# Kernel tuning notes

Measured on AMD Instinct MI355X. Metric: run time of the kernel, lower is better.

The kernel has to match this reference:

```python
import jax, jax.numpy as jnp
import numpy as np

B, C, H, W = 4, 256, 96, 96
HEADS, RATE = 8, 1


def setup_inputs() -> dict:
    key = jax.random.key(0)
    ks = [jax.random.fold_in(key, i) for i in range(8)]
    kpe = 2 * (RATE // 2) + 1  # PE depthwise kernel size (1 for rate=1)
    return {
        "q": jax.random.normal(ks[0], (B, C, H, W), jnp.float32),
        "k": jax.random.normal(ks[1], (B, C, H, W), jnp.float32),
        "v": jax.random.normal(ks[2], (B, C, H, W), jnp.float32),
        "wq": jax.random.normal(ks[3], (C, C), jnp.float32) * 0.02,          # q_proj 1x1 (used for q,k,v per source)
        "pe_dw": jax.random.normal(ks[4], (9, 1, kpe, kpe), jnp.float32) * 0.3,  # grouped conv, groups=9
        "pe_pw": jax.random.normal(ks[5], (9, 9, 1, 1), jnp.float32) * 0.3,      # 1x1 mixing conv
        "wo": jax.random.normal(ks[6], (C, C), jnp.float32) * 0.02,          # out_proj weight
        "bo": jax.random.normal(ks[7], (C,), jnp.float32) * 0.02,            # out_proj bias
    }


def _unfold3(x, rate):
    # torch.nn.Unfold(3, dilation=rate, padding=rate) then view(N, c, 9, H, W)
    # kernel positions are row-major (ki, kj), channel-major layout -> stack on axis 2.
    n, c, h, w = x.shape
    xp = jnp.pad(x, ((0, 0), (0, 0), (rate, rate), (rate, rate)))
    pats = [xp[:, :, i * rate:i * rate + h, j * rate:j * rate + w]
            for i in range(3) for j in range(3)]
    return jnp.stack(pats, axis=2)  # (N, c, 9, H, W)


def reference(q, b_unused_k=None, v=None, wq=None, pe_dw=None, pe_pw=None, wo=None, bo=None, k=None):
    raise NotImplementedError  # replaced below


def reference(q, k, v, wq, pe_dw, pe_pw, wo, bo):
    b = q.shape[0]
    ch = C // HEADS
    proj = lambda x: jnp.einsum('oc,bchw->bohw', wq, x)  # source uses q_proj for q, k AND v
    qh = proj(q).reshape(b * HEADS, ch, H, W)
    kh = proj(k).reshape(b * HEADS, ch, H, W)
    vh = proj(v).reshape(b * HEADS, ch, H, W)

    ku = _unfold3(kh, RATE)                              # (bH, ch, 9, H, W)
    f = jnp.einsum('nchw,nckhw->nkhw', qh, ku)           # per-pixel 3x3 scores (bH, 9, H, W)

    pad = RATE // 2
    dn = ('NCHW', 'OIHW', 'NCHW')
    f = jax.lax.conv_general_dilated(f, pe_dw, (1, 1), [(pad, pad), (pad, pad)],
                                     feature_group_count=9, dimension_numbers=dn)
    f = jax.lax.conv_general_dilated(f, pe_pw, (1, 1), 'VALID', dimension_numbers=dn)
    s = jax.nn.softmax(f, axis=1)                        # softmax over 9 kernel positions

    vu = _unfold3(vh, RATE)                              # (bH, ch, 9, H, W)
    o = jnp.einsum('nckhw,nkhw->nchw', vu, s).reshape(b, C, H, W)
    return jnp.einsum('oc,bchw->bohw', wo, o) + bo[None, :, None, None]
```

## Files before the change

### kernel.cpp

```cpp
#include <hip/hip_runtime.h>
#include <math.h>

#define HH 96
#define WW 96
#define PP 9216
#define CCH 256
#define BB 4
#define CH 32

typedef unsigned short u16;
typedef short bf16x8 __attribute__((ext_vector_type(8)));
typedef float f32x4 __attribute__((ext_vector_type(4)));

__device__ __forceinline__ float bf2f(unsigned s) { return __uint_as_float(s << 16); }
__device__ __forceinline__ u16 f2bf(float f) {
  unsigned u = __float_as_uint(f);
  return (u16)((u + 0x7fffu + ((u >> 16) & 1u)) >> 16);
}

typedef __attribute__((address_space(1))) const unsigned int GUI;
typedef __attribute__((address_space(3))) unsigned int LUI;
__device__ __forceinline__ void gload16(const void* g, void* l) {
  __builtin_amdgcn_global_load_lds((GUI*)g, (LUI*)l, 16, 0, 0);
}

__global__ __launch_bounds__(256)
void wcvt(const float* __restrict__ wq, const float* __restrict__ wo,
          u16* __restrict__ Wbf) {
  int i = blockIdx.x * 256 + threadIdx.x;
  const float* s = (i < 16384) ? (wq + (size_t)i * 4) : (wo + (size_t)(i - 16384) * 4);
  float4 v = *(const float4*)s;
  uint2 u;
  u.x = (unsigned)f2bf(v.x) | ((unsigned)f2bf(v.y) << 16);
  u.y = (unsigned)f2bf(v.z) | ((unsigned)f2bf(v.w) << 16);
  *(uint2*)(Wbf + (size_t)i * 4) = u;
}

__global__ __launch_bounds__(256)
void gemm_qkvf(const float* __restrict__ qin, const float* __restrict__ kin,
               const float* __restrict__ vin, const u16* __restrict__ Wbf,
               u16* __restrict__ Xcl) {
  __shared__ u16 Wl[256 * 64];
  __shared__ u16 Xl[64 * 64];
  const int t = threadIdx.x;
  const int w = t >> 6, l = t & 63;
  const int lr = l & 15, lg = l >> 4;
  const int pblk = blockIdx.x * 64;
  const int z = blockIdx.z;
  const int b = z & 3, which = z >> 2;
  const float* Xf = ((which == 0) ? qin : (which == 1) ? kin : vin) + (size_t)b * CCH * PP;
  u16* Y = Xcl + (size_t)z * ((size_t)PP * CCH);

  f32x4 acc[4][4];
#pragma unroll
  for (int mi = 0; mi < 4; mi++)
#pragma unroll
    for (int ni = 0; ni < 4; ni++) acc[mi][ni] = (f32x4){0.f, 0.f, 0.f, 0.f};

  for (int kk = 0; kk < 4; kk++) {
    const int c0 = kk * 64;
#pragma unroll
    for (int i = 0; i < 8; i++) {
      int r0 = (w * 8 + i) * 8;
      int row = r0 + (l >> 3);
      int gs = (l & 7) ^ (row & 7);
      gload16(Wbf + (size_t)row * CCH + c0 + gs * 8, (void*)&Wl[r0 * 64]);
    }
    float4 xr[4];
#pragma unroll
    for (int rr = 0; rr < 4; rr++) {
      int cc = w * 4 + rr * 16 + lg;
      xr[rr] = *(const float4*)(Xf + (size_t)(c0 + cc) * PP + pblk + lr * 4);
    }
#pragma unroll
    for (int rr = 0; rr < 4; rr++) {
      float r0 = xr[rr].x, r1 = xr[rr].y, r2 = xr[rr].z, r3 = xr[rr].w;
      bool b0 = (lg & 1), b1 = (lg & 2);
      float s0 = b0 ? r0 : r1;
      float s1 = b0 ? r2 : r3;
      float u0 = __shfl_xor(s0, 16, 64);
      float u1 = __shfl_xor(s1, 16, 64);
      float m0 = b0 ? u0 : r0;
      float m1 = b0 ? r1 : u0;
      float m2 = b0 ? u1 : r2;
      float m3 = b0 ? r3 : u1;
      float s2 = b1 ? m0 : m2;
      float s3 = b1 ? m1 : m3;
      float w0 = __shfl_xor(s2, 32, 64);
      float w1 = __shfl_xor(s3, 32, 64);
      float o0 = b1 ? w0 : m0;
      float o1 = b1 ? w1 : m1;
      float o2 = b1 ? m2 : w0;
      float o3 = b1 ? m3 : w1;
      int cbase = w * 4 + rr * 16;
      int pl = lr * 4 + lg;
      int qg = cbase >> 3, h8 = (cbase >> 2) & 1;
      unsigned lo = (unsigned)f2bf(o0) | ((unsigned)f2bf(o1) << 16);
      unsigned hi = (unsigned)f2bf(o2) | ((unsigned)f2bf(o3) << 16);
      *(uint2*)(&Xl[pl * 64 + ((qg ^ (pl & 7)) << 3) + h8 * 4]) = make_uint2(lo, hi);
    }
    __syncthreads();
#pragma unroll
    for (int ks = 0; ks < 2; ks++) {
      const int g = ks * 4 + lg;
      bf16x8 wf[4], xf[4];
#pragma unroll
      for (int i = 0; i < 4; i++) {
        int row = w * 64 + i * 16 + lr;
        wf[i] = *(const bf16x8*)&Wl[row * 64 + ((g ^ (row & 7)) << 3)];
      }
#pragma unroll
      for (int i = 0; i < 4; i++) {
        int row = i * 16 + lr;
        xf[i] = *(const bf16x8*)&Xl[row * 64 + ((g ^ (row & 7)) << 3)];
      }
#pragma unroll
      for (int mi = 0; mi < 4; mi++)
#pragma unroll
        for (int ni = 0; ni < 4; ni++)
          acc[mi][ni] = __builtin_amdgcn_mfma_f32_16x16x32_bf16(
              wf[mi], xf[ni], acc[mi][ni], 0, 0, 0);
    }
    __syncthreads();
  }
#pragma unroll
  for (int mi = 0; mi < 4; mi++)
#pragma unroll
    for (int ni = 0; ni < 4; ni++) {
      int o = w * 64 + mi * 16 + lg * 4;
      int p = pblk + ni * 16 + lr;
      f32x4 a = acc[mi][ni];
      uint2 u;
      u.x = (unsigned)f2bf(a[0]) | ((unsigned)f2bf(a[1]) << 16);
      u.y = (unsigned)f2bf(a[2]) | ((unsigned)f2bf(a[3]) << 16);
      *(uint2*)(Y + (size_t)p * CCH + o) = u;
    }
}

__global__ __launch_bounds__(256)
void gemm_out_m(const u16* __restrict__ Xbuf, const u16* __restrict__ Wbf,
                const float* __restrict__ bias, float* __restrict__ outY) {
  __shared__ u16 Wl[256 * 64];
  __shared__ u16 Xl[64 * 64];
  const int t = threadIdx.x;
  const int w = t >> 6, l = t & 63;
  const int lr = l & 15, lg = l >> 4;
  const int pblk = blockIdx.x * 64;
  const int z = blockIdx.z;
  const u16* Xb = Xbuf + (size_t)z * ((size_t)PP * CCH);

  f32x4 acc[4][4];
#pragma unroll
  for (int mi = 0; mi < 4; mi++)
#pragma unroll
    for (int ni = 0; ni < 4; ni++) acc[mi][ni] = (f32x4){0.f, 0.f, 0.f, 0.f};

  for (int kk = 0; kk < 4; kk++) {
    const int c0 = kk * 64;
#pragma unroll
    for (int i = 0; i < 8; i++) {
      int r0 = (w * 8 + i) * 8;
      int row = r0 + (l >> 3);
      int gs = (l & 7) ^ (row & 7);
      gload16(Wbf + (size_t)row * CCH + c0 + gs * 8, (void*)&Wl[r0 * 64]);
    }
#pragma unroll
    for (int i = 0; i < 2; i++) {
      int r0 = (w * 2 + i) * 8;
      int row = r0 + (l >> 3);
      int gs = (l & 7) ^ (row & 7);
      gload16(Xb + (size_t)(pblk + row) * CCH + c0 + gs * 8, (void*)&Xl[r0 * 64]);
    }
    __syncthreads();
#pragma unroll
    for (int ks = 0; ks < 2; ks++) {
      const int g = ks * 4 + lg;
      bf16x8 wf[4], xf[4];
#pragma unroll
      for (int i = 0; i < 4; i++) {
        int row = w * 64 + i * 16 + lr;
        wf[i] = *(const bf16x8*)&Wl[row * 64 + ((g ^ (row & 7)) << 3)];
      }
#pragma unroll
      for (int i = 0; i < 4; i++) {
        int row = i * 16 + lr;
        xf[i] = *(const bf16x8*)&Xl[row * 64 + ((g ^ (row & 7)) << 3)];
      }
#pragma unroll
      for (int mi = 0; mi < 4; mi++)
#pragma unroll
        for (int ni = 0; ni < 4; ni++)
          acc[mi][ni] = __builtin_amdgcn_mfma_f32_16x16x32_bf16(
              xf[mi], wf[ni], acc[mi][ni], 0, 0, 0);
    }
    __syncthreads();
  }
#pragma unroll
  for (int ni = 0; ni < 4; ni++) {
    int o = w * 64 + ni * 16 + lr;
    float bv = bias[o];
#pragma unroll
    for (int mi = 0; mi < 4; mi++) {
      int p = pblk + mi * 16 + lg * 4;
      f32x4 a = acc[mi][ni];
      float4 st = {a[0] + bv, a[1] + bv, a[2] + bv, a[3] + bv};
      *(float4*)(outY + ((size_t)z * CCH + o) * PP + p) = st;
    }
  }
}

#define TX 32
#define TY 4
#define HX 34
#define HY 6
#define NHP (HX * HY)
#define NGR (NHP * 4)
#define ARND 4

__device__ __forceinline__ void fma8(const uint4 u, const float* qp, float& s) {
  s = fmaf(qp[0], bf2f(u.x & 0xffffu), s);
  s = fmaf(qp[1], bf2f(u.x >> 16), s);
  s = fmaf(qp[2], bf2f(u.y & 0xffffu), s);
  s = fmaf(qp[3], bf2f(u.y >> 16), s);
  s = fmaf(qp[4], bf2f(u.z & 0xffffu), s);
  s = fmaf(qp[5], bf2f(u.z >> 16), s);
  s = fmaf(qp[6], bf2f(u.w & 0xffffu), s);
  s = fmaf(qp[7], bf2f(u.w >> 16), s);
}
__device__ __forceinline__ void acc8(const uint4 u, float gv, float* op) {
  op[0] = fmaf(gv, bf2f(u.x & 0xffffu), op[0]);
  op[1] = fmaf(gv, bf2f(u.x >> 16), op[1]);
  op[2] = fmaf(gv, bf2f(u.y & 0xffffu), op[2]);
  op[3] = fmaf(gv, bf2f(u.y >> 16), op[3]);
  op[4] = fmaf(gv, bf2f(u.z & 0xffffu), op[4]);
  op[5] = fmaf(gv, bf2f(u.z >> 16), op[5]);
  op[6] = fmaf(gv, bf2f(u.w & 0xffffu), op[6]);
  op[7] = fmaf(gv, bf2f(u.w >> 16), op[7]);
}

__global__ __launch_bounds__(256)
void attn_1b(const u16* __restrict__ Kt, const u16* __restrict__ Vt,
             u16* __restrict__ Qt, const float* __restrict__ pe_dw,
             const float* __restrict__ pe_pw) {
  __shared__ __align__(16) u16 kl[NHP * 32];
  __shared__ __align__(16) u16 vl[NHP * 32];
  __shared__ float coef[81];
  const int t = threadIdx.x;
  if (t < 81) coef[t] = pe_pw[t] * pe_dw[t % 9];

  const int lx = t & 31;
  const int h2 = (t >> 5) & 1;
  const int ly = t >> 6;
  const int x0 = blockIdx.x * TX;
  const int y0 = blockIdx.y * TY;
  const int b = blockIdx.z >> 3;
  const int h = blockIdx.z & 7;
  const size_t nbase = (size_t)b * PP * CCH + h * CH;
  const int p = (y0 + ly) * WW + (x0 + lx);
  const size_t pixhalf = nbase + (size_t)p * CCH + h2 * 16;

  uint4 kg[ARND], vg[ARND];
#pragma unroll
  for (int r = 0; r < ARND; r++) {
    int s = t + r * 256;
    int pix = s >> 2, g = s & 3;
    int hy = pix / HX, hx = pix - hy * HX;
    int gx = x0 - 1 + hx, gy = y0 - 1 + hy;
    bool ok = (s < NGR) & (gx >= 0) & (gx < WW) & (gy >= 0) & (gy < HH);
    uint4 u = make_uint4(0u, 0u, 0u, 0u);
    if (ok) u = *(const uint4*)(Kt + nbase + (size_t)(gy * WW + gx) * CCH + g * 8);
    kg[r] = u;
  }
#pragma unroll
  for (int r = 0; r < ARND; r++) {
    int s = t + r * 256;
    int pix = s >> 2, g = s & 3;
    int hy = pix / HX, hx = pix - hy * HX;
    int gx = x0 - 1 + hx, gy = y0 - 1 + hy;
    bool ok = (s < NGR) & (gx >= 0) & (gx < WW) & (gy >= 0) & (gy < HH);
    uint4 u = make_uint4(0u, 0u, 0u, 0u);
    if (ok) u = *(const uint4*)(Vt + nbase + (size_t)(gy * WW + gx) * CCH + g * 8);
    vg[r] = u;
  }
  uint4 q0 = *(const uint4*)(Qt + pixhalf);
  uint4 q1 = *(const uint4*)(Qt + pixhalf + 8);

#pragma unroll
  for (int r = 0; r < ARND; r++) {
    int s = t + r * 256;
    if (s < NGR) {
      int pix = s >> 2, g = s & 3;
      *(uint4*)(&kl[pix * 32 + (((g + (pix >> 1)) & 3) << 3)]) = kg[r];
    }
  }
#pragma unroll
  for (int r = 0; r < ARND; r++) {
    int s = t + r * 256;
    if (s < NGR) {
      int pix = s >> 2, g = s & 3;
      *(uint4*)(&vl[pix * 32 + (((g + (pix >> 1)) & 3) << 3)]) = vg[r];
    }
  }
  __syncthreads();

  float qh[16];
  qh[0] = bf2f(q0.x & 0xffffu); qh[1] = bf2f(q0.x >> 16);
  qh[2] = bf2f(q0.y & 0xffffu); qh[3] = bf2f(q0.y >> 16);
  qh[4] = bf2f(q0.z & 0xffffu); qh[5] = bf2f(q0.z >> 16);
  qh[6] = bf2f(q0.w & 0xffffu); qh[7] = bf2f(q0.w >> 16);
  qh[8] = bf2f(q1.x & 0xffffu); qh[9] = bf2f(q1.x >> 16);
  qh[10] = bf2f(q1.y & 0xffffu); qh[11] = bf2f(q1.y >> 16);
  qh[12] = bf2f(q1.z & 0xffffu); qh[13] = bf2f(q1.z >> 16);
  qh[14] = bf2f(q1.w & 0xffffu); qh[15] = bf2f(q1.w >> 16);

  float f[9];
#pragma unroll
  for (int kk = 0; kk < 9; kk++) {
    int pix = (ly + kk / 3) * HX + lx + kk % 3;
    int ga = h2 * 2;
    uint4 ka = *(const uint4*)(&kl[pix * 32 + (((ga + (pix >> 1)) & 3) << 3)]);
    uint4 kb = *(const uint4*)(&kl[pix * 32 + (((ga + 1 + (pix >> 1)) & 3) << 3)]);
    float s = 0.f;
    fma8(ka, qh, s);
    fma8(kb, qh + 8, s);
    f[kk] = s + __shfl_xor(s, 32, 64);
  }

  float g[9], m = -1e30f;
#pragma unroll
  for (int k2 = 0; k2 < 9; k2++) {
    float s = 0.f;
#pragma unroll
    for (int kk = 0; kk < 9; kk++) s = fmaf(coef[k2 * 9 + kk], f[kk], s);
    g[k2] = s;
    m = fmaxf(m, s);
  }
  float ssum = 0.f;
#pragma unroll
  for (int k2 = 0; k2 < 9; k2++) {
    g[k2] = __expf(g[k2] - m);
    ssum += g[k2];
  }
  float inv = 1.f / ssum;
#pragma unroll
  for (int k2 = 0; k2 < 9; k2++) g[k2] *= inv;

  float oh[16];
#pragma unroll
  for (int j = 0; j < 16; j++) oh[j] = 0.f;
#pragma unroll
  for (int kk = 0; kk < 9; kk++) {
    int pix = (ly + kk / 3) * HX + lx + kk % 3;
    int ga = h2 * 2;
    uint4 va = *(const uint4*)(&vl[pix * 32 + (((ga + (pix >> 1)) & 3) << 3)]);
    uint4 vb = *(const uint4*)(&vl[pix * 32 + (((ga + 1 + (pix >> 1)) & 3) << 3)]);
    acc8(va, g[kk], oh);
    acc8(vb, g[kk], oh + 8);
  }
  uint4 s0, s1;
  s0.x = (unsigned)f2bf(oh[0]) | ((unsigned)f2bf(oh[1]) << 16);
  s0.y = (unsigned)f2bf(oh[2]) | ((unsigned)f2bf(oh[3]) << 16);
  s0.z = (unsigned)f2bf(oh[4]) | ((unsigned)f2bf(oh[5]) << 16);
  s0.w = (unsigned)f2bf(oh[6]) | ((unsigned)f2bf(oh[7]) << 16);
  s1.x = (unsigned)f2bf(oh[8]) | ((unsigned)f2bf(oh[9]) << 16);
  s1.y = (unsigned)f2bf(oh[10]) | ((unsigned)f2bf(oh[11]) << 16);
  s1.z = (unsigned)f2bf(oh[12]) | ((unsigned)f2bf(oh[13]) << 16);
  s1.w = (unsigned)f2bf(oh[14]) | ((unsigned)f2bf(oh[15]) << 16);
  *(uint4*)(Qt + pixhalf) = s0;
  *(uint4*)(Qt + pixhalf + 8) = s1;
}

extern "C" void kernel_launch(void* const* d_in, const int* in_sizes, int n_in,
                              void* d_out, int out_size, void* d_ws, size_t ws_size,
                              hipStream_t stream) {
  const float* q     = (const float*)d_in[0];
  const float* k     = (const float*)d_in[1];
  const float* v     = (const float*)d_in[2];
  const float* wq    = (const float*)d_in[3];
  const float* pe_dw = (const float*)d_in[4];
  const float* pe_pw = (const float*)d_in[5];
  const float* wo    = (const float*)d_in[6];
  const float* bo    = (const float*)d_in[7];
  float* out = (float*)d_out;

  const size_t seg = (size_t)BB * PP * CCH;
  u16* Xcl = (u16*)d_ws;
  u16* Wbf = Xcl + 3 * seg;

  wcvt<<<128, 256, 0, stream>>>(wq, wo, Wbf);

  gemm_qkvf<<<dim3(PP / 64, 1, 12), 256, 0, stream>>>(q, k, v, Wbf, Xcl);

  u16* Qs = Xcl;
  u16* Ks = Xcl + seg;
  u16* Vs = Xcl + 2 * seg;
  attn_1b<<<dim3(WW / TX, HH / TY, BB * 8), 256, 0, stream>>>(Ks, Vs, Qs, pe_dw, pe_pw);

  gemm_out_m<<<dim3(PP / 64, 1, BB), 256, 0, stream>>>(Qs, Wbf + 65536, bo, out);
}
```

Baseline: 95.40 us.

## Pre-swizzle weights into MFMA fragment order and double-buffer fp32 input tile

The weight conversion kernel now writes bf16 weights pre-arranged in per-lane MFMA fragment order, so both GEMMs read weight fragments straight from global memory and no longer stage them in shared memory. The QKV projection GEMM stores the fp32 input tile transposed into a double-buffered, XOR-swizzled LDS buffer and converts to bf16 at fragment-read time. It prefetches the next K slice while the MFMAs run, which removes one barrier per iteration, and sets launch bounds to 3 blocks per SM. In exchange, weight fragments now come from global or L2 memory on every k-step instead of LDS, and the fp32 LDS tile adds conversion ALU work.

```diff
diff --git a/kernel.cpp b/kernel.cpp
--- a/kernel.cpp
+++ b/kernel.cpp
@@ -27,21 +27,34 @@
 __global__ __launch_bounds__(256)
 void wcvt(const float* __restrict__ wq, const float* __restrict__ wo,
           u16* __restrict__ Wbf) {
-  int i = blockIdx.x * 256 + threadIdx.x;
-  const float* s = (i < 16384) ? (wq + (size_t)i * 4) : (wo + (size_t)(i - 16384) * 4);
-  float4 v = *(const float4*)s;
-  uint2 u;
-  u.x = (unsigned)f2bf(v.x) | ((unsigned)f2bf(v.y) << 16);
-  u.y = (unsigned)f2bf(v.z) | ((unsigned)f2bf(v.w) << 16);
-  *(uint2*)(Wbf + (size_t)i * 4) = u;
-}
-
-__global__ __launch_bounds__(256)
+  int gidx = blockIdx.x * 256 + threadIdx.x;
+  int mat = gidx >> 13;
+  int gi = gidx & 8191;
+  int l = gi & 63;
+  int i = (gi >> 6) & 3;
+  int w = (gi >> 8) & 3;
+  int ks = (gi >> 10) & 1;
+  int kk = (gi >> 11) & 3;
+  const float* W = mat ? wo : wq;
+  int row = w * 64 + i * 16 + (l & 15);
+  int c0 = kk * 64 + (ks * 4 + (l >> 4)) * 8;
+  const float* s = W + (size_t)row * CCH + c0;
+  float4 a = *(const float4*)s;
+  float4 b = *(const float4*)(s + 4);
+  uint4 u;
+  u.x = (unsigned)f2bf(a.x) | ((unsigned)f2bf(a.y) << 16);
+  u.y = (unsigned)f2bf(a.z) | ((unsigned)f2bf(a.w) << 16);
+  u.z = (unsigned)f2bf(b.x) | ((unsigned)f2bf(b.y) << 16);
+  u.w = (unsigned)f2bf(b.z) | ((unsigned)f2bf(b.w) << 16);
+  *(uint4*)(Wbf + (size_t)gidx * 8) = u;
+}
+
+#define TSTR 68
+__global__ __launch_bounds__(256, 3)
 void gemm_qkvf(const float* __restrict__ qin, const float* __restrict__ kin,
                const float* __restrict__ vin, const u16* __restrict__ Wbf,
                u16* __restrict__ Xcl) {
-  __shared__ u16 Wl[256 * 64];
-  __shared__ u16 Xl[64 * 64];
+  __shared__ float Tt[2][64][TSTR];
   const int t = threadIdx.x;
   const int w = t >> 6, l = t & 63;
   const int lr = l & 15, lg = l >> 4;
@@ -51,68 +64,55 @@
   const float* Xf = ((which == 0) ? qin : (which == 1) ? kin : vin) + (size_t)b * CCH * PP;
   u16* Y = Xcl + (size_t)z * ((size_t)PP * CCH);
 
+  const int sw_r = ((lr >> 2) & 3) << 3;
+  const int cswz = (lr & 3) << 3;
+
   f32x4 acc[4][4];
 #pragma unroll
   for (int mi = 0; mi < 4; mi++)
 #pragma unroll
     for (int ni = 0; ni < 4; ni++) acc[mi][ni] = (f32x4){0.f, 0.f, 0.f, 0.f};
 
-  for (int kk = 0; kk < 4; kk++) {
-    const int c0 = kk * 64;
-#pragma unroll
-    for (int i = 0; i < 8; i++) {
-      int r0 = (w * 8 + i) * 8;
-      int row = r0 + (l >> 3);
-      int gs = (l & 7) ^ (row & 7);
-      gload16(Wbf + (size_t)row * CCH + c0 + gs * 8, (void*)&Wl[r0 * 64]);
-    }
-    float4 xr[4];
+  float4 xr[4];
+  auto loadX = [&](int kk) {
 #pragma unroll
     for (int rr = 0; rr < 4; rr++) {
-      int cc = w * 4 + rr * 16 + lg;
-      xr[rr] = *(const float4*)(Xf + (size_t)(c0 + cc) * PP + pblk + lr * 4);
-    }
+      int cc = kk * 64 + w * 4 + lg + 16 * rr;
+      xr[rr] = *(const float4*)(Xf + (size_t)cc * PP + pblk + lr * 4);
+    }
+  };
+  auto writeT = [&](int buf) {
 #pragma unroll
     for (int rr = 0; rr < 4; rr++) {
-      float r0 = xr[rr].x, r1 = xr[rr].y, r2 = xr[rr].z, r3 = xr[rr].w;
-      bool b0 = (lg & 1), b1 = (lg & 2);
-      float s0 = b0 ? r0 : r1;
-      float s1 = b0 ? r2 : r3;
-      float u0 = __shfl_xor(s0, 16, 64);
-      float u1 = __shfl_xor(s1, 16, 64);
-      float m0 = b0 ? u0 : r0;
-      float m1 = b0 ? r1 : u0;
-      float m2 = b0 ? u1 : r2;
-      float m3 = b0 ? r3 : u1;
-      float s2 = b1 ? m0 : m2;
-      float s3 = b1 ? m1 : m3;
-      float w0 = __shfl_xor(s2, 32, 64);
-      float w1 = __shfl_xor(s3, 32, 64);
-      float o0 = b1 ? w0 : m0;
-      float o1 = b1 ? w1 : m1;
-      float o2 = b1 ? m2 : w0;
-      float o3 = b1 ? m3 : w1;
-      int cbase = w * 4 + rr * 16;
-      int pl = lr * 4 + lg;
-      int qg = cbase >> 3, h8 = (cbase >> 2) & 1;
-      unsigned lo = (unsigned)f2bf(o0) | ((unsigned)f2bf(o1) << 16);
-      unsigned hi = (unsigned)f2bf(o2) | ((unsigned)f2bf(o3) << 16);
-      *(uint2*)(&Xl[pl * 64 + ((qg ^ (pl & 7)) << 3) + h8 * 4]) = make_uint2(lo, hi);
-    }
-    __syncthreads();
+      int cs = (w * 4 + lg + 16 * rr) ^ cswz;
+      Tt[buf][lr * 4 + 0][cs] = xr[rr].x;
+      Tt[buf][lr * 4 + 1][cs] = xr[rr].y;
+      Tt[buf][lr * 4 + 2][cs] = xr[rr].z;
+      Tt[buf][lr * 4 + 3][cs] = xr[rr].w;
+    }
+  };
+  auto mma = [&](int kk, int cur) {
 #pragma unroll
     for (int ks = 0; ks < 2; ks++) {
-      const int g = ks * 4 + lg;
       bf16x8 wf[4], xf[4];
 #pragma unroll
       for (int i = 0; i < 4; i++) {
-        int row = w * 64 + i * 16 + lr;
-        wf[i] = *(const bf16x8*)&Wl[row * 64 + ((g ^ (row & 7)) << 3)];
+        size_t go = ((((size_t)(kk * 2 + ks) * 4 + w) * 4 + i) * 64 + l) * 8;
+        wf[i] = *(const bf16x8*)(Wbf + go);
       }
 #pragma unroll
       for (int i = 0; i < 4; i++) {
         int row = i * 16 + lr;
-        xf[i] = *(const bf16x8*)&Xl[row * 64 + ((g ^ (row & 7)) << 3)];
+        int c0 = (ks * 32 + lg * 8) ^ sw_r;
+        const float* tp = &Tt[cur][row][c0];
+        float4 A = *(const float4*)tp;
+        float4 Bv = *(const float4*)(tp + 4);
+        bf16x8 x;
+        x[0] = (short)f2bf(A.x);  x[1] = (short)f2bf(A.y);
+        x[2] = (short)f2bf(A.z);  x[3] = (short)f2bf(A.w);
+        x[4] = (short)f2bf(Bv.x); x[5] = (short)f2bf(Bv.y);
+        x[6] = (short)f2bf(Bv.z); x[7] = (short)f2bf(Bv.w);
+        xf[i] = x;
       }
 #pragma unroll
       for (int mi = 0; mi < 4; mi++)
@@ -121,8 +121,21 @@
           acc[mi][ni] = __builtin_amdgcn_mfma_f32_16x16x32_bf16(
               wf[mi], xf[ni], acc[mi][ni], 0, 0, 0);
     }
-    __syncthreads();
-  }
+  };
+
+  loadX(0);
+  writeT(0);
+  __syncthreads();
+#pragma unroll
+  for (int kk = 0; kk < 4; kk++) {
+    if (kk < 3) loadX(kk + 1);
+    mma(kk, kk & 1);
+    if (kk < 3) {
+      writeT((kk + 1) & 1);
+      __syncthreads();
+    }
+  }
+
 #pragma unroll
   for (int mi = 0; mi < 4; mi++)
 #pragma unroll
@@ -140,7 +153,6 @@
 __global__ __launch_bounds__(256)
 void gemm_out_m(const u16* __restrict__ Xbuf, const u16* __restrict__ Wbf,
                 const float* __restrict__ bias, float* __restrict__ outY) {
-  __shared__ u16 Wl[256 * 64];
   __shared__ u16 Xl[64 * 64];
   const int t = threadIdx.x;
   const int w = t >> 6, l = t & 63;
@@ -158,13 +170,6 @@
   for (int kk = 0; kk < 4; kk++) {
     const int c0 = kk * 64;
 #pragma unroll
-    for (int i = 0; i < 8; i++) {
-      int r0 = (w * 8 + i) * 8;
-      int row = r0 + (l >> 3);
-      int gs = (l & 7) ^ (row & 7);
-      gload16(Wbf + (size_t)row * CCH + c0 + gs * 8, (void*)&Wl[r0 * 64]);
-    }
-#pragma unroll
     for (int i = 0; i < 2; i++) {
       int r0 = (w * 2 + i) * 8;
       int row = r0 + (l >> 3);
@@ -178,8 +183,8 @@
       bf16x8 wf[4], xf[4];
 #pragma unroll
       for (int i = 0; i < 4; i++) {
-        int row = w * 64 + i * 16 + lr;
-        wf[i] = *(const bf16x8*)&Wl[row * 64 + ((g ^ (row & 7)) << 3)];
+        size_t go = ((((size_t)(kk * 2 + ks) * 4 + w) * 4 + i) * 64 + l) * 8;
+        wf[i] = *(const bf16x8*)(Wbf + go);
       }
 #pragma unroll
       for (int i = 0; i < 4; i++) {
@@ -387,7 +392,7 @@
   u16* Xcl = (u16*)d_ws;
   u16* Wbf = Xcl + 3 * seg;
 
-  wcvt<<<128, 256, 0, stream>>>(wq, wo, Wbf);
+  wcvt<<<64, 256, 0, stream>>>(wq, wo, Wbf);
 
   gemm_qkvf<<<dim3(PP / 64, 1, 12), 256, 0, stream>>>(q, k, v, Wbf, Xcl);
 
```

New measurement: 96.40 us. No clear change (+1.1%).
